# Optimization experiments

Hardware: AMD Instinct MI355X
Metric: run time of the kernel (lower is better)

The kernel has to match this reference:

```python
import jax, jax.numpy as jnp
import numpy as np

B, I, E, X, T, W = 32768, 512, 8, 128, 2, 64


def setup_inputs() -> dict:
    key = jax.random.key(0)
    ks = jax.random.split(key, 6)
    sc = lambda k, shape, s: (jax.random.normal(k, shape, jnp.float32) * s)
    return {
        "x": jax.random.normal(ks[0], (B, I), jnp.float32),
        "We": sc(ks[1], (E, I, X), 0.04),       # per-expert SLP weights
        "be": jnp.zeros((E, X), jnp.float32),
        "gates": sc(ks[2], (T, I, E), 0.04),    # per-task gating matrices (no softmax in original)
        "tW1": sc(ks[3], (T, X, W), 0.08),      # tower MLP layer 1
        "tb1": jnp.zeros((T, W), jnp.float32),
        "tW2": sc(ks[4], (T, W, 1), 0.1),       # tower MLP layer 2 (scalar head)
        "tb2": jnp.zeros((T, 1), jnp.float32),
    }


def reference(x, We, be, gates, tW1, tb1, tW2, tb2):
    # task gates: [T, B, E] (raw matmul, faithful to original: no softmax applied)
    g = jnp.einsum('bi,tie->tbe', x, gates)
    # expert SLPs (Linear + ReLU): [E, B, X]
    ex = jax.nn.relu(jnp.einsum('bi,eix->ebx', x, We) + be[:, None, :])
    # fused replacement of the nested expert_size x num_experts loop:
    # shared_info[t, b, i] = sum_j g[t,b,j] * ex[j,b,i]
    shared = jnp.einsum('tbe,ebx->tbx', g, ex)
    # tower MLPs: Linear -> ReLU -> Linear(1)
    h = jax.nn.relu(jnp.einsum('tbx,txw->tbw', shared, tW1) + tb1[:, None, :])
    out = jnp.einsum('tbw,two->tbo', h, tW2) + tb2[:, None, :]
    return out  # [T, B, 1], row t = task t's output
```

## Files before the change

kernel.cpp:

```cpp
#include <hip/hip_runtime.h>
#include <cstdint>
#include <cstddef>

#define NB 32768
#define KI 512
#define NE 8
#define NX 128
#define NT 2
#define NWD 64
#define BM 128
#define THREADS 512
#define SMEM_BYTES 163840

#define W2_ELEMS (NE * KI * NX)
#define G2_OFF   W2_ELEMS
#define G2_ELEMS (64 * 16 * 8)
#define T2_OFF   (G2_OFF + G2_ELEMS)
#define T2_ELEMS (NT * 16 * 64 * 8)
#define WS_NEED  ((size_t)(W2_ELEMS + G2_ELEMS + T2_ELEMS) * 2)

typedef __attribute__((ext_vector_type(8))) short bf16x8;
typedef __attribute__((ext_vector_type(4))) float f32x4;

__device__ __forceinline__ unsigned short f2bf(float f) {
  union { float f; unsigned u; } v; v.f = f;
  return (unsigned short)((v.u + 0x7fffu + ((v.u >> 16) & 1u)) >> 16);
}

#define AS1(p) ((const __attribute__((address_space(1))) void*)(uintptr_t)(p))
#define AS3(p) ((__attribute__((address_space(3))) void*)(uintptr_t)(p))
#define VMCNT2() asm volatile("s_waitcnt vmcnt(2)" ::: "memory")
#define BAR()    __builtin_amdgcn_s_barrier()

__global__ __launch_bounds__(256) void repack_we_kernel(const float* __restrict__ We,
                                                        unsigned short* __restrict__ ws) {
  int tid = blockIdx.x * 256 + threadIdx.x;
  int col  = tid & (NX - 1);
  int kblk = (tid >> 7) & 63;
  int e    = tid >> 13;
  const float* src = We + ((size_t)e * KI + (size_t)kblk * 8) * NX + col;
  bf16x8 v;
#pragma unroll
  for (int j = 0; j < 8; ++j) v[j] = (short)f2bf(src[(size_t)j * NX]);
  *(bf16x8*)(ws + (size_t)tid * 8) = v;
}

__global__ __launch_bounds__(256) void repack_aux_kernel(const float* __restrict__ gates,
                                                         const float* __restrict__ tW1,
                                                         unsigned short* __restrict__ ws) {
  int tid = threadIdx.x;
#pragma unroll
  for (int i = 0; i < 4; ++i) {
    int f = i * 256 + tid;
    int kb = f >> 4, col = f & 15;
    int t = col >> 3, e = col & 7;
    const float* src = gates + (size_t)t * (KI * NE) + (size_t)(kb * 8) * NE + e;
    bf16x8 v;
#pragma unroll
    for (int j = 0; j < 8; ++j) v[j] = (short)f2bf(src[(size_t)j * NE]);
    *(bf16x8*)(ws + G2_OFF + (size_t)f * 8) = v;
  }
#pragma unroll
  for (int i = 0; i < 8; ++i) {
    int f = i * 256 + tid;
    int t = f >> 10, kb = (f >> 6) & 15, col = f & 63;
    const float* src = tW1 + (size_t)t * (NX * NWD) + (size_t)(kb * 8) * NWD + col;
    bf16x8 v;
#pragma unroll
    for (int j = 0; j < 8; ++j) v[j] = (short)f2bf(src[(size_t)j * NWD]);
    *(bf16x8*)(ws + T2_OFF + (size_t)f * 8) = v;
  }
}

template <bool USE_WS>
__global__ __launch_bounds__(THREADS, 2)
void moe_fused_kernel(const float* __restrict__ x, const float* __restrict__ We,
                      const float* __restrict__ be, const float* __restrict__ gates,
                      const float* __restrict__ tW1, const float* __restrict__ tb1,
                      const float* __restrict__ tW2, const float* __restrict__ tb2,
                      const unsigned short* __restrict__ ws, float* __restrict__ out) {
  extern __shared__ char smem[];
  char* wbuf = smem + 131072;

  const int tid  = threadIdx.x;
  const int lane = tid & 63;
  const int wid  = tid >> 6;
  const int l15  = lane & 15;
  const int lhi  = lane >> 4;
  const int row0 = blockIdx.x * BM;

  {
    const float4* xs4 = (const float4*)(x + (size_t)row0 * KI);
#pragma unroll
    for (int c = 0; c < 16; ++c) {
      int i = c * THREADS + tid;
      float4 a0 = xs4[(size_t)i * 2];
      float4 a1 = xs4[(size_t)i * 2 + 1];
      bf16x8 v;
      v[0] = (short)f2bf(a0.x); v[1] = (short)f2bf(a0.y);
      v[2] = (short)f2bf(a0.z); v[3] = (short)f2bf(a0.w);
      v[4] = (short)f2bf(a1.x); v[5] = (short)f2bf(a1.y);
      v[6] = (short)f2bf(a1.z); v[7] = (short)f2bf(a1.w);
      int row = i >> 6;
      int kb  = (i & 63) * 16;
      *(bf16x8*)(smem + row * 1024 + (kb ^ ((row & 7) << 4))) = v;
    }
  }
  __syncthreads();

  const int arow = wid * 16 + l15;
  char* abase = smem + arow * 1024;
  const int asw = (arow & 7) << 4;
  auto loadA = [&](int kk, int ks) -> bf16x8 {
    return *(const bf16x8*)(abase + ((kk * 128 + ks * 64 + lhi * 16) ^ asw));
  };

  auto stage_w = [&](int e, int kk, int b) {
    if constexpr (USE_WS) {
      const char* gbase = (const char*)ws + ((size_t)(e * 64 + kk * 8) * NX) * 16;
      char* lbase = wbuf + b * 16384 + wid * 1024;
      __builtin_amdgcn_global_load_lds(AS1(gbase + (wid * 64 + lane) * 16), AS3(lbase), 16, 0, 0);
      __builtin_amdgcn_global_load_lds(AS1(gbase + 8192 + (wid * 64 + lane) * 16), AS3(lbase + 8192), 16, 0, 0);
    } else {
      const int col = tid & 127;
      const int kb0 = tid >> 7;
#pragma unroll
      for (int h = 0; h < 2; ++h) {
        const int kblk = kb0 + h * 4;
        const float* src = We + ((size_t)e * KI + (size_t)(kk * 64 + kblk * 8)) * NX + col;
        bf16x8 v;
#pragma unroll
        for (int j = 0; j < 8; ++j) v[j] = (short)f2bf(src[(size_t)j * NX]);
        *(bf16x8*)(wbuf + b * 16384 + (kblk * NX + col) * 16) = v;
      }
    }
  };

  f32x4 acc[8];
  f32x4 shacc[NT][8];
  f32x4 gacc = {0.f, 0.f, 0.f, 0.f};
#pragma unroll
  for (int t = 0; t < NT; ++t)
#pragma unroll
    for (int cf = 0; cf < 8; ++cf) shacc[t][cf] = (f32x4){0.f, 0.f, 0.f, 0.f};

  float be_r[NE][8];
#pragma unroll
  for (int e = 0; e < NE; ++e)
#pragma unroll
    for (int cf = 0; cf < 8; ++cf) be_r[e][cf] = be[e * NX + cf * 16 + l15];

  stage_w(0, 0, 0);
  {
#pragma unroll
    for (int gks = 0; gks < 16; ++gks) {
      bf16x8 gb;
      if constexpr (USE_WS) {
        gb = *(const bf16x8*)(ws + G2_OFF + ((size_t)(gks * 4 + lhi) * 16 + l15) * 8);
      } else {
        int t = l15 >> 3, e = l15 & 7;
        const float* src = gates + (size_t)t * (KI * NE) + (size_t)((gks * 4 + lhi) * 8) * NE + e;
#pragma unroll
        for (int j = 0; j < 8; ++j) gb[j] = (short)f2bf(src[(size_t)j * NE]);
      }
      gacc = __builtin_amdgcn_mfma_f32_16x16x32_bf16(loadA(gks >> 1, gks & 1), gb, gacc, 0, 0, 0);
    }
  }

  for (int e = 0; e < NE; ++e) {
#pragma unroll
    for (int cf = 0; cf < 8; ++cf) acc[cf] = (f32x4){0.f, 0.f, 0.f, 0.f};
#pragma unroll
    for (int kk = 0; kk < 8; ++kk) {
      const int ne_ = (kk == 7) ? ((e + 1) & 7) : e;
      const int nk  = (kk + 1) & 7;
      stage_w(ne_, nk, (kk + 1) & 1);
      if constexpr (USE_WS) { VMCNT2(); BAR(); } else { __syncthreads(); }
#pragma unroll
      for (int ks = 0; ks < 2; ++ks) {
        bf16x8 av = loadA(kk, ks);
        const char* bbase = wbuf + (kk & 1) * 16384 + ((ks * 4 + lhi) * NX + l15) * 16;
#pragma unroll
        for (int cf = 0; cf < 8; ++cf) {
          bf16x8 bfr = *(const bf16x8*)(bbase + cf * 256);
          acc[cf] = __builtin_amdgcn_mfma_f32_16x16x32_bf16(av, bfr, acc[cf], 0, 0, 0);
        }
      }
      if constexpr (USE_WS) { BAR(); } else { __syncthreads(); }
    }
    {
      float gv0[4], gv1[4];
#pragma unroll
      for (int r = 0; r < 4; ++r) {
        gv0[r] = __shfl(gacc[r], (lane & 48) | e, 64);
        gv1[r] = __shfl(gacc[r], (lane & 48) | (8 + e), 64);
      }
#pragma unroll
      for (int cf = 0; cf < 8; ++cf) {
        const float bev = be_r[e][cf];
#pragma unroll
        for (int r = 0; r < 4; ++r) {
          float ex = fmaxf(acc[cf][r] + bev, 0.f);
          shacc[0][cf][r] += gv0[r] * ex;
          shacc[1][cf][r] += gv1[r] * ex;
        }
      }
    }
  }

  __syncthreads();
#pragma unroll
  for (int t = 0; t < NT; ++t)
#pragma unroll
    for (int cf = 0; cf < 8; ++cf)
#pragma unroll
      for (int r = 0; r < 4; ++r) {
        const int rr = wid * 16 + lhi * 4 + r;
        const int cc = cf * 16 + l15;
        *(unsigned short*)(smem + t * 32768 + rr * 256 + ((cc * 2) ^ ((rr & 7) << 4))) =
            f2bf(shacc[t][cf][r]);
      }
  __syncthreads();

  const int trow = wid * 16 + l15;
  const char* tbase = smem + trow * 256;
  const int tsw = (trow & 7) << 4;
#pragma unroll
  for (int t = 0; t < NT; ++t) {
    f32x4 hacc[4];
#pragma unroll
    for (int cf = 0; cf < 4; ++cf) hacc[cf] = (f32x4){0.f, 0.f, 0.f, 0.f};
#pragma unroll
    for (int ks = 0; ks < 4; ++ks) {
      bf16x8 a = *(const bf16x8*)(tbase + t * 32768 + ((ks * 64 + lhi * 16) ^ tsw));
#pragma unroll
      for (int cf = 0; cf < 4; ++cf) {
        bf16x8 bv;
        if constexpr (USE_WS) {
          bv = *(const bf16x8*)(ws + T2_OFF + ((size_t)(t * 16 + ks * 4 + lhi) * 64 + cf * 16 + l15) * 8);
        } else {
          const float* src = tW1 + (size_t)t * (NX * NWD) + (size_t)((ks * 4 + lhi) * 8) * NWD + cf * 16 + l15;
#pragma unroll
          for (int j = 0; j < 8; ++j) bv[j] = (short)f2bf(src[(size_t)j * NWD]);
        }
        hacc[cf] = __builtin_amdgcn_mfma_f32_16x16x32_bf16(a, bv, hacc[cf], 0, 0, 0);
      }
    }
    float p[4] = {0.f, 0.f, 0.f, 0.f};
#pragma unroll
    for (int cf = 0; cf < 4; ++cf) {
      int col = cf * 16 + l15;
      const float b1v = tb1[t * NWD + col];
      const float w2v = tW2[t * NWD + col];
#pragma unroll
      for (int r = 0; r < 4; ++r) p[r] += fmaxf(hacc[cf][r] + b1v, 0.f) * w2v;
    }
#pragma unroll
    for (int r = 0; r < 4; ++r) {
      p[r] += __shfl_xor(p[r], 1, 64);
      p[r] += __shfl_xor(p[r], 2, 64);
      p[r] += __shfl_xor(p[r], 4, 64);
      p[r] += __shfl_xor(p[r], 8, 64);
    }
    if (l15 == 0) {
      const float b2 = tb2[t];
      float4 o;
      o.x = p[0] + b2; o.y = p[1] + b2; o.z = p[2] + b2; o.w = p[3] + b2;
      *(float4*)(out + (size_t)t * NB + row0 + wid * 16 + lhi * 4) = o;
    }
  }
}

extern "C" void kernel_launch(void* const* d_in, const int* in_sizes, int n_in,
                              void* d_out, int out_size, void* d_ws, size_t ws_size,
                              hipStream_t stream) {
  const float* x     = (const float*)d_in[0];
  const float* We    = (const float*)d_in[1];
  const float* be    = (const float*)d_in[2];
  const float* gates = (const float*)d_in[3];
  const float* tW1   = (const float*)d_in[4];
  const float* tb1   = (const float*)d_in[5];
  const float* tW2   = (const float*)d_in[6];
  const float* tb2   = (const float*)d_in[7];
  float* out = (float*)d_out;

  const bool use_ws = (d_ws != nullptr) && (ws_size >= WS_NEED);
  const int nblk = NB / BM;

  if (use_ws) {
    unsigned short* ws = (unsigned short*)d_ws;
    hipFuncSetAttribute(reinterpret_cast<const void*>(moe_fused_kernel<true>),
                        hipFuncAttributeMaxDynamicSharedMemorySize, SMEM_BYTES);
    repack_we_kernel<<<(W2_ELEMS / 8) / 256, 256, 0, stream>>>(We, ws);
    repack_aux_kernel<<<1, 256, 0, stream>>>(gates, tW1, ws);
    moe_fused_kernel<true><<<nblk, THREADS, SMEM_BYTES, stream>>>(
        x, We, be, gates, tW1, tb1, tW2, tb2, ws, out);
  } else {
    hipFuncSetAttribute(reinterpret_cast<const void*>(moe_fused_kernel<false>),
                        hipFuncAttributeMaxDynamicSharedMemorySize, SMEM_BYTES);
    moe_fused_kernel<false><<<nblk, THREADS, SMEM_BYTES, stream>>>(
        x, We, be, gates, tW1, tb1, tW2, tb2, nullptr, out);
  }
}
```

Before: 70.14 us.

## Retile expert GEMM with 32x32 MFMA, 2x4 wave grid and 4-stage weight ring

Restructures the expert GEMM so each wave computes a 64x64 tile with 32x32x16 bf16 MFMAs over paired experts. Waves are arranged 2x4 and stream 8KB weight chunks through a 4-deep LDS ring buffer, and the repacked weight layout changes to match. The goal is to raise operand reuse per LDS read and to cut the number of barriers and loads per MFMA. Because each wave covers a column half of one expert pair, the per-task shared outputs of the two expert halves are combined through LDS in two passes. This adds an extra bf16 rounding of the partial sums and extra readlane work for the gate values.

```diff
diff --git a/kernel.cpp b/kernel.cpp
--- a/kernel.cpp
+++ b/kernel.cpp
@@ -11,6 +11,8 @@
 #define BM 128
 #define THREADS 512
 #define SMEM_BYTES 163840
+#define WOFF   131072
+#define CHUNK_B 8192
 
 #define W2_ELEMS (NE * KI * NX)
 #define G2_OFF   W2_ELEMS
@@ -21,10 +23,17 @@
 
 typedef __attribute__((ext_vector_type(8))) short bf16x8;
 typedef __attribute__((ext_vector_type(4))) float f32x4;
+typedef __attribute__((ext_vector_type(16))) float f32x16;
+
+#define ZERO16 (f32x16){0.f,0.f,0.f,0.f,0.f,0.f,0.f,0.f,0.f,0.f,0.f,0.f,0.f,0.f,0.f,0.f}
 
 __device__ __forceinline__ unsigned short f2bf(float f) {
   union { float f; unsigned u; } v; v.f = f;
   return (unsigned short)((v.u + 0x7fffu + ((v.u >> 16) & 1u)) >> 16);
+}
+__device__ __forceinline__ float bf2f(unsigned short u) {
+  union { unsigned u; float f; } v; v.u = ((unsigned)u) << 16;
+  return v.f;
 }
 
 #define AS1(p) ((const __attribute__((address_space(1))) void*)(uintptr_t)(p))
@@ -34,15 +43,17 @@
 
 __global__ __launch_bounds__(256) void repack_we_kernel(const float* __restrict__ We,
                                                         unsigned short* __restrict__ ws) {
-  int tid = blockIdx.x * 256 + threadIdx.x;
-  int col  = tid & (NX - 1);
-  int kblk = (tid >> 7) & 63;
-  int e    = tid >> 13;
-  const float* src = We + ((size_t)e * KI + (size_t)kblk * 8) * NX + col;
+  int F = blockIdx.x * 256 + threadIdx.x;
+  int col = F & 255;
+  int kb  = (F >> 8) & 1;
+  int kc  = (F >> 9) & 31;
+  int n   = F >> 14;
+  int e   = 2 * n + (col >> 7);
+  const float* src = We + ((size_t)e * KI + (size_t)(kc * 16 + kb * 8)) * NX + (col & 127);
   bf16x8 v;
 #pragma unroll
   for (int j = 0; j < 8; ++j) v[j] = (short)f2bf(src[(size_t)j * NX]);
-  *(bf16x8*)(ws + (size_t)tid * 8) = v;
+  *(bf16x8*)(ws + (size_t)F * 8) = v;
 }
 
 __global__ __launch_bounds__(256) void repack_aux_kernel(const float* __restrict__ gates,
@@ -80,13 +91,17 @@
                       const float* __restrict__ tW2, const float* __restrict__ tb2,
                       const unsigned short* __restrict__ ws, float* __restrict__ out) {
   extern __shared__ char smem[];
-  char* wbuf = smem + 131072;
+  char* wbuf = smem + WOFF;
 
   const int tid  = threadIdx.x;
   const int lane = tid & 63;
   const int wid  = tid >> 6;
   const int l15  = lane & 15;
   const int lhi  = lane >> 4;
+  const int l31  = lane & 31;
+  const int h    = lane >> 5;
+  const int wr   = wid >> 2;
+  const int wc   = wid & 3;
   const int row0 = blockIdx.x * BM;
 
   {
@@ -108,50 +123,31 @@
   }
   __syncthreads();
 
-  const int arow = wid * 16 + l15;
-  char* abase = smem + arow * 1024;
-  const int asw = (arow & 7) << 4;
-  auto loadA = [&](int kk, int ks) -> bf16x8 {
-    return *(const bf16x8*)(abase + ((kk * 128 + ks * 64 + lhi * 16) ^ asw));
+  auto stage_w = [&](int cc) {
+    if constexpr (USE_WS) {
+      const char* gb = (const char*)ws + (size_t)cc * CHUNK_B;
+      char* lb = wbuf + (cc & 3) * CHUNK_B + wid * 1024;
+      __builtin_amdgcn_global_load_lds(AS1(gb + (wid * 64 + lane) * 16), AS3(lb), 16, 0, 0);
+    } else {
+      const int n = cc >> 5, kc = cc & 31;
+      const int col = tid & 255, kb = tid >> 8;
+      const int e = 2 * n + (col >> 7);
+      const float* src = We + ((size_t)e * KI + (size_t)(kc * 16 + kb * 8)) * NX + (col & 127);
+      bf16x8 v;
+#pragma unroll
+      for (int j = 0; j < 8; ++j) v[j] = (short)f2bf(src[(size_t)j * NX]);
+      *(bf16x8*)(wbuf + (cc & 3) * CHUNK_B + tid * 16) = v;
+    }
   };
 
-  auto stage_w = [&](int e, int kk, int b) {
-    if constexpr (USE_WS) {
-      const char* gbase = (const char*)ws + ((size_t)(e * 64 + kk * 8) * NX) * 16;
-      char* lbase = wbuf + b * 16384 + wid * 1024;
-      __builtin_amdgcn_global_load_lds(AS1(gbase + (wid * 64 + lane) * 16), AS3(lbase), 16, 0, 0);
-      __builtin_amdgcn_global_load_lds(AS1(gbase + 8192 + (wid * 64 + lane) * 16), AS3(lbase + 8192), 16, 0, 0);
-    } else {
-      const int col = tid & 127;
-      const int kb0 = tid >> 7;
-#pragma unroll
-      for (int h = 0; h < 2; ++h) {
-        const int kblk = kb0 + h * 4;
-        const float* src = We + ((size_t)e * KI + (size_t)(kk * 64 + kblk * 8)) * NX + col;
-        bf16x8 v;
-#pragma unroll
-        for (int j = 0; j < 8; ++j) v[j] = (short)f2bf(src[(size_t)j * NX]);
-        *(bf16x8*)(wbuf + b * 16384 + (kblk * NX + col) * 16) = v;
-      }
-    }
-  };
-
-  f32x4 acc[8];
-  f32x4 shacc[NT][8];
-  f32x4 gacc = {0.f, 0.f, 0.f, 0.f};
-#pragma unroll
-  for (int t = 0; t < NT; ++t)
-#pragma unroll
-    for (int cf = 0; cf < 8; ++cf) shacc[t][cf] = (f32x4){0.f, 0.f, 0.f, 0.f};
-
-  float be_r[NE][8];
-#pragma unroll
-  for (int e = 0; e < NE; ++e)
-#pragma unroll
-    for (int cf = 0; cf < 8; ++cf) be_r[e][cf] = be[e * NX + cf * 16 + l15];
-
-  stage_w(0, 0, 0);
+  stage_w(0);
+  stage_w(1);
+
+  const int asw = (lane & 7) << 4;
+
+  f32x4 g16[4] = {{0.f,0.f,0.f,0.f},{0.f,0.f,0.f,0.f},{0.f,0.f,0.f,0.f},{0.f,0.f,0.f,0.f}};
   {
+    const char* abg = smem + (wr * 64 + l15) * 1024;
 #pragma unroll
     for (int gks = 0; gks < 16; ++gks) {
       bf16x8 gb;
@@ -163,63 +159,100 @@
 #pragma unroll
         for (int j = 0; j < 8; ++j) gb[j] = (short)f2bf(src[(size_t)j * NE]);
       }
-      gacc = __builtin_amdgcn_mfma_f32_16x16x32_bf16(loadA(gks >> 1, gks & 1), gb, gacc, 0, 0, 0);
-    }
-  }
-
-  for (int e = 0; e < NE; ++e) {
-#pragma unroll
-    for (int cf = 0; cf < 8; ++cf) acc[cf] = (f32x4){0.f, 0.f, 0.f, 0.f};
-#pragma unroll
-    for (int kk = 0; kk < 8; ++kk) {
-      const int ne_ = (kk == 7) ? ((e + 1) & 7) : e;
-      const int nk  = (kk + 1) & 7;
-      stage_w(ne_, nk, (kk + 1) & 1);
+      const int ao = (gks * 64 + lhi * 16) ^ asw;
+#pragma unroll
+      for (int rfg = 0; rfg < 4; ++rfg)
+        g16[rfg] = __builtin_amdgcn_mfma_f32_16x16x32_bf16(
+            *(const bf16x8*)(abg + rfg * 16384 + ao), gb, g16[rfg], 0, 0, 0);
+    }
+  }
+
+  float be_r[4][2];
+#pragma unroll
+  for (int n = 0; n < 4; ++n)
+#pragma unroll
+    for (int cf = 0; cf < 2; ++cf)
+      be_r[n][cf] = be[(2 * n + (wc >> 1)) * NX + (wc & 1) * 64 + cf * 32 + l31];
+
+  f32x16 shacc[NT][2][2];
+#pragma unroll
+  for (int t = 0; t < NT; ++t)
+#pragma unroll
+    for (int rf = 0; rf < 2; ++rf)
+#pragma unroll
+      for (int cf = 0; cf < 2; ++cf) shacc[t][rf][cf] = ZERO16;
+
+  const char* abase0 = smem + (wr * 64 + l31) * 1024;
+  const char* abase1 = abase0 + 32 * 1024;
+  const int boff0 = (h * 256 + wc * 64 + l31) * 16;
+
+#pragma unroll
+  for (int n = 0; n < 4; ++n) {
+    f32x16 acc[2][2];
+    acc[0][0] = ZERO16; acc[0][1] = ZERO16; acc[1][0] = ZERO16; acc[1][1] = ZERO16;
+#pragma unroll 4
+    for (int kc = 0; kc < 32; ++kc) {
+      const int c = n * 32 + kc;
+      stage_w((c + 2) & 127);
       if constexpr (USE_WS) { VMCNT2(); BAR(); } else { __syncthreads(); }
-#pragma unroll
-      for (int ks = 0; ks < 2; ++ks) {
-        bf16x8 av = loadA(kk, ks);
-        const char* bbase = wbuf + (kk & 1) * 16384 + ((ks * 4 + lhi) * NX + l15) * 16;
-#pragma unroll
-        for (int cf = 0; cf < 8; ++cf) {
-          bf16x8 bfr = *(const bf16x8*)(bbase + cf * 256);
-          acc[cf] = __builtin_amdgcn_mfma_f32_16x16x32_bf16(av, bfr, acc[cf], 0, 0, 0);
+      const char* bb = wbuf + (c & 3) * CHUNK_B;
+      const int ao = (kc * 32 + h * 16) ^ asw;
+      bf16x8 a0 = *(const bf16x8*)(abase0 + ao);
+      bf16x8 a1 = *(const bf16x8*)(abase1 + ao);
+      bf16x8 b0 = *(const bf16x8*)(bb + boff0);
+      bf16x8 b1 = *(const bf16x8*)(bb + boff0 + 512);
+      acc[0][0] = __builtin_amdgcn_mfma_f32_32x32x16_bf16(a0, b0, acc[0][0], 0, 0, 0);
+      acc[0][1] = __builtin_amdgcn_mfma_f32_32x32x16_bf16(a0, b1, acc[0][1], 0, 0, 0);
+      acc[1][0] = __builtin_amdgcn_mfma_f32_32x32x16_bf16(a1, b0, acc[1][0], 0, 0, 0);
+      acc[1][1] = __builtin_amdgcn_mfma_f32_32x32x16_bf16(a1, b1, acc[1][1], 0, 0, 0);
+    }
+    {
+      const int ew = __builtin_amdgcn_readfirstlane(2 * n + (wc >> 1));
+#pragma unroll
+      for (int rf = 0; rf < 2; ++rf)
+#pragma unroll
+        for (int reg = 0; reg < 16; ++reg) {
+          const int f  = rf * 2 + (reg >> 3);
+          const int r  = reg & 3;
+          const int b0i = 32 * ((reg >> 2) & 1);
+          int vi = __float_as_int(g16[f][r]);
+          float g00 = __int_as_float(__builtin_amdgcn_readlane(vi, ew + b0i));
+          float g01 = __int_as_float(__builtin_amdgcn_readlane(vi, ew + b0i + 16));
+          float g10 = __int_as_float(__builtin_amdgcn_readlane(vi, ew + b0i + 8));
+          float g11 = __int_as_float(__builtin_amdgcn_readlane(vi, ew + b0i + 24));
+          float gv0 = h ? g01 : g00;
+          float gv1 = h ? g11 : g10;
+          float ex0 = fmaxf(acc[rf][0][reg] + be_r[n][0], 0.f);
+          float ex1 = fmaxf(acc[rf][1][reg] + be_r[n][1], 0.f);
+          shacc[0][rf][0][reg] += gv0 * ex0;
+          shacc[0][rf][1][reg] += gv0 * ex1;
+          shacc[1][rf][0][reg] += gv1 * ex0;
+          shacc[1][rf][1][reg] += gv1 * ex1;
         }
-      }
-      if constexpr (USE_WS) { BAR(); } else { __syncthreads(); }
-    }
-    {
-      float gv0[4], gv1[4];
-#pragma unroll
-      for (int r = 0; r < 4; ++r) {
-        gv0[r] = __shfl(gacc[r], (lane & 48) | e, 64);
-        gv1[r] = __shfl(gacc[r], (lane & 48) | (8 + e), 64);
-      }
-#pragma unroll
-      for (int cf = 0; cf < 8; ++cf) {
-        const float bev = be_r[e][cf];
-#pragma unroll
-        for (int r = 0; r < 4; ++r) {
-          float ex = fmaxf(acc[cf][r] + bev, 0.f);
-          shacc[0][cf][r] += gv0[r] * ex;
-          shacc[1][cf][r] += gv1[r] * ex;
-        }
-      }
     }
   }
 
   __syncthreads();
-#pragma unroll
-  for (int t = 0; t < NT; ++t)
-#pragma unroll
-    for (int cf = 0; cf < 8; ++cf)
-#pragma unroll
-      for (int r = 0; r < 4; ++r) {
-        const int rr = wid * 16 + lhi * 4 + r;
-        const int cc = cf * 16 + l15;
-        *(unsigned short*)(smem + t * 32768 + rr * 256 + ((cc * 2) ^ ((rr & 7) << 4))) =
-            f2bf(shacc[t][cf][r]);
-      }
+  auto sh_io = [&](bool combine) {
+#pragma unroll
+    for (int t = 0; t < NT; ++t)
+#pragma unroll
+      for (int rf = 0; rf < 2; ++rf)
+#pragma unroll
+        for (int cf = 0; cf < 2; ++cf)
+#pragma unroll
+          for (int reg = 0; reg < 16; ++reg) {
+            int row = wr * 64 + rf * 32 + (reg & 3) + 8 * (reg >> 2) + 4 * h;
+            int col = (wc & 1) * 64 + cf * 32 + l31;
+            char* p = smem + t * 32768 + row * 256 + ((col * 2) ^ ((row & 7) << 4));
+            float v = shacc[t][rf][cf][reg];
+            if (combine) v += bf2f(*(unsigned short*)p);
+            *(unsigned short*)p = f2bf(v);
+          }
+  };
+  if (wc < 2) sh_io(false);
+  __syncthreads();
+  if (wc >= 2) sh_io(true);
   __syncthreads();
 
   const int trow = wid * 16 + l15;
```

Result: slower. 99.79 us (+42.3%).
